# Kernel tuning notes

Hardware: AMD Instinct MI355X
Metric: run time of the kernel (lower is better)

Reference implementation:

```python
import jax, jax.numpy as jnp
import numpy as np

WS = (2, 8, 8)      # window size (wt, wh, ww)
SS = (1, 4, 4)      # shift size
HEADS = 6


def _window_partition(x, ws):
    B, T, H, W, C = x.shape
    wt, wh, ww = ws
    x = x.reshape(B, T // wt, wt, H // wh, wh, W // ww, ww, C)
    x = x.transpose(0, 1, 3, 5, 2, 4, 6, 7)
    return x.reshape(-1, wt * wh * ww, C)  # (B*nW, N, C)


def _window_reverse(w, ws, B, T, H, W):
    wt, wh, ww = ws
    C = w.shape[-1]
    x = w.reshape(B, T // wt, H // wh, W // ww, wt, wh, ww, C)
    x = x.transpose(0, 1, 4, 2, 5, 3, 6, 7)
    return x.reshape(B, T, H, W, C)


def _rel_pos_index(ws):
    wt, wh, ww = ws
    coords = np.stack(np.meshgrid(np.arange(wt), np.arange(wh), np.arange(ww), indexing='ij'))
    coords = coords.reshape(3, -1)                      # (3, N)
    rel = coords[:, :, None] - coords[:, None, :]       # (3, N, N)
    rel = rel.transpose(1, 2, 0).astype(np.int32)
    rel[..., 0] += wt - 1
    rel[..., 1] += wh - 1
    rel[..., 2] += ww - 1
    rel[..., 0] *= (2 * wh - 1) * (2 * ww - 1)
    rel[..., 1] *= (2 * ww - 1)
    return rel.sum(-1)                                  # (N, N)


def _shift_mask(T, H, W, ws, ss):
    # standard Swin shifted-window attention mask
    img = np.zeros((1, T, H, W, 1), dtype=np.float32)
    cnt = 0
    for t in (slice(0, -ws[0]), slice(-ws[0], -ss[0]), slice(-ss[0], None)):
        for h in (slice(0, -ws[1]), slice(-ws[1], -ss[1]), slice(-ss[1], None)):
            for w in (slice(0, -ws[2]), slice(-ws[2], -ss[2]), slice(-ss[2], None)):
                img[:, t, h, w, :] = cnt
                cnt += 1
    mw = np.asarray(_window_partition(jnp.asarray(img), ws)).squeeze(-1)  # (nW, N)
    diff = mw[:, None, :] - mw[:, :, None]
    return jnp.asarray(np.where(diff != 0, -100.0, 0.0).astype(np.float32))


def setup_inputs() -> dict:
    key = jax.random.key(0)
    ks = jax.random.split(key, 9)
    B, T, H, W, C = 2, 8, 64, 64, 192
    hid = 4 * C
    s = 0.02
    x = jax.random.normal(ks[0], (B, T, H, W, C), jnp.float32)
    qkv_w = jax.random.normal(ks[1], (3 * C, C), jnp.float32) * s
    qkv_b = jnp.zeros((3 * C,), jnp.float32)
    proj_w = jax.random.normal(ks[2], (C, C), jnp.float32) * s
    proj_b = jnp.zeros((C,), jnp.float32)
    n_rel = (2 * WS[0] - 1) * (2 * WS[1] - 1) * (2 * WS[2] - 1)
    rpb_table = jax.random.normal(ks[3], (n_rel, HEADS), jnp.float32) * s
    rpb_index = jnp.asarray(_rel_pos_index(WS))
    fc1_w = jax.random.normal(ks[4], (hid, C), jnp.float32) * s
    fc1_b = jnp.zeros((hid,), jnp.float32)
    fc2_w = jax.random.normal(ks[5], (C, hid), jnp.float32) * s
    fc2_b = jnp.zeros((C,), jnp.float32)
    attn_mask = _shift_mask(T, H, W, WS, SS)
    return dict(x=x, attn_mask=attn_mask, qkv_w=qkv_w, qkv_b=qkv_b, proj_w=proj_w,
                proj_b=proj_b, rpb_table=rpb_table, rpb_index=rpb_index,
                fc1_w=fc1_w, fc1_b=fc1_b, fc2_w=fc2_w, fc2_b=fc2_b)


def reference(x, attn_mask, qkv_w, qkv_b, proj_w, proj_b, rpb_table, rpb_index,
              fc1_w, fc1_b, fc2_w, fc2_b):
    B, T, H, W, C = x.shape
    h = HEADS
    d = C // h
    scale = d ** -0.5

    shifted = jnp.roll(x, (-SS[0], -SS[1], -SS[2]), axis=(1, 2, 3))
    xw = _window_partition(shifted, WS)            # (Bn, N, C)
    Bn, N, _ = xw.shape

    qkv = (xw @ qkv_w.T + qkv_b).reshape(Bn, N, 3, h, d).transpose(2, 0, 3, 1, 4)
    q, k, v = qkv[0], qkv[1], qkv[2]               # (Bn, h, N, d)
    attn = jnp.einsum('bhnd,bhmd->bhnm', q * scale, k)
    bias = rpb_table[rpb_index.reshape(-1)].reshape(N, N, h).transpose(2, 0, 1)
    attn = attn + bias[None]
    nW = attn_mask.shape[0]
    attn = (attn.reshape(Bn // nW, nW, h, N, N) + attn_mask[None, :, None]).reshape(Bn, h, N, N)
    attn = jax.nn.softmax(attn, axis=-1)
    out = jnp.einsum('bhnm,bhmd->bhnd', attn, v).transpose(0, 2, 1, 3).reshape(Bn, N, C)
    out = out @ proj_w.T + proj_b

    z = _window_reverse(out, WS, B, T, H, W)
    z = jnp.roll(z, (SS[0], SS[1], SS[2]), axis=(1, 2, 3))

    y = z + x
    mlp = jax.nn.gelu(y @ fc1_w.T + fc1_b, approximate=False) @ fc2_w.T + fc2_b
    return x + mlp
```

## Files before the change

### kernel.cpp

```cpp
#include <hip/hip_runtime.h>
#include <hip/hip_bf16.h>

typedef __attribute__((ext_vector_type(4))) float f32x4;
typedef __attribute__((ext_vector_type(8))) short bf16x8;

#define DEV __device__ __forceinline__

DEV unsigned short f2bf(float f) {
  union { float f; unsigned int u; } v; v.f = f;
  unsigned int r = v.u + 0x7fffu + ((v.u >> 16) & 1u);
  return (unsigned short)(r >> 16);
}

DEV float bf2f(unsigned short u) {
  union { unsigned int u; float f; } v; v.u = ((unsigned int)u) << 16; return v.f;
}

DEV short2 pkbf(float a, float b) {
  float2 t; t.x = a; t.y = b;
  __hip_bfloat162 h = __float22bfloat162_rn(t);
  union { __hip_bfloat162 h; short2 s; } u; u.h = h; return u.s;
}

DEV bf16x8 cvt8(float4 u, float4 v) {
  short2 a = pkbf(u.x, u.y), b = pkbf(u.z, u.w), c = pkbf(v.x, v.y), d = pkbf(v.z, v.w);
  bf16x8 r;
  r[0] = a.x; r[1] = a.y; r[2] = b.x; r[3] = b.y;
  r[4] = c.x; r[5] = c.y; r[6] = d.x; r[7] = d.y;
  return r;
}

DEV float gelu_fast(float v) {
  float u = 1.5957691216057308f * v * (1.0f + 0.044715f * v * v);
  return v * __builtin_amdgcn_rcpf(1.0f + __expf(-u));
}

DEV size_t winmap(int row) {
  int wIdx = row >> 7, n = row & 127;
  int b = wIdx >> 8, widx = wIdx & 255;
  int t = (((widx >> 6) * 2 + (n >> 6)) + 1) & 7;
  int h = ((((widx >> 3) & 7) * 8 + ((n >> 3) & 7)) + 4) & 63;
  int w = (((widx & 7) * 8 + (n & 7)) + 4) & 63;
  return (size_t)(((b * 8 + t) * 64 + h) * 64 + w);
}

DEV int reg3(int tw, int hw, int ww, int n) {
  int ts = tw * 2 + (n >> 6);
  int hs = hw * 8 + ((n >> 3) & 7);
  int wsv = ww * 8 + (n & 7);
  int rt = (ts >= 7) ? 2 : ((ts >= 6) ? 1 : 0);
  int rh = (hs >= 60) ? 2 : ((hs >= 56) ? 1 : 0);
  int rw = (wsv >= 60) ? 2 : ((wsv >= 56) ? 1 : 0);
  return rt * 9 + rh * 3 + rw;
}

DEV void gload16(const unsigned short* g, unsigned short* lds) {
  __builtin_amdgcn_global_load_lds(
      (const __attribute__((address_space(1))) unsigned int*)g,
      (__attribute__((address_space(3))) unsigned int*)lds, 16, 0, 0);
}

__global__ __launch_bounds__(256) void k_prep(
    const float* __restrict__ qkv_w, const float* __restrict__ proj_w,
    const float* __restrict__ fc1_w, const float* __restrict__ fc2_w,
    const float* __restrict__ rpb_t, const int* __restrict__ rpb_i,
    unsigned short* __restrict__ wq, unsigned short* __restrict__ wp,
    unsigned short* __restrict__ w1, unsigned short* __restrict__ w2,
    float* __restrict__ b6) {
  int i = blockIdx.x * 256 + threadIdx.x;
  if (i < 110592) wq[i] = f2bf(qkv_w[i]);
  if (i < 36864)  wp[i] = f2bf(proj_w[i]);
  if (i < 147456) { w1[i] = f2bf(fc1_w[i]); w2[i] = f2bf(fc2_w[i]); }
  if (i < 16384) {
    int row = i >> 7, col = i & 127;
    int idx = rpb_i[i];
    int dest = (row >> 4) * 2048 + (((row >> 2) & 3) * 16 + (col & 15)) * 32 +
               (col >> 4) * 4 + (row & 3);
    #pragma unroll
    for (int h = 0; h < 6; ++h) b6[h * 16384 + dest] = rpb_t[idx * 6 + h];
  }
}

__global__ __launch_bounds__(256) void k_qkv(
    const float* __restrict__ x, const unsigned short* __restrict__ Bm,
    const float* __restrict__ bias, unsigned short* __restrict__ outb) {
  __shared__ char smem[40960];
  float* As = (float*)smem;
  unsigned short* Bs = (unsigned short*)(smem + 32768);
  unsigned short* Cs = (unsigned short*)smem;
  const int tid = threadIdx.x;
  const int wave = tid >> 6, lane = tid & 63;
  const int lin = ((int)blockIdx.x & 7) * 576 + ((int)blockIdx.x >> 3);
  const int mt = lin / 9, nt = lin - mt * 9;
  const int m0 = mt * 128, n0 = nt * 64;
  const int wr = wave >> 1, wc = wave & 1;
  const int l8 = lane >> 3, s8 = lane & 7;

  const float* aptr[8];
  #pragma unroll
  for (int i = 0; i < 8; ++i) {
    int row = wave * 32 + i * 4 + (lane >> 4);
    aptr[i] = x + winmap(m0 + row) * 192 + (((lane & 15) ^ (row & 15)) << 2);
  }

  f32x4 acc[4][2] = {};
  for (int kt = 0; kt < 192; kt += 64) {
    __syncthreads();
    #pragma unroll
    for (int i = 0; i < 8; ++i)
      gload16((const unsigned short*)(aptr[i] + kt), (unsigned short*)(As + (wave * 8 + i) * 256));
    #pragma unroll
    for (int j = 0; j < 2; ++j) {
      int c = wave * 2 + j;
      int row = c * 8 + l8;
      gload16(Bm + (size_t)(n0 + row) * 192 + kt + (s8 ^ l8) * 8, Bs + c * 512);
    }
    __syncthreads();

    #pragma unroll
    for (int kk = 0; kk < 2; ++kk) {
      bf16x8 af[4], bfr[2];
      #pragma unroll
      for (int mi = 0; mi < 4; ++mi) {
        int r = wr * 64 + mi * 16 + (lane & 15);
        int s0 = kk * 8 + (lane >> 4) * 2;
        float4 u = *(const float4*)(As + r * 64 + ((s0 ^ (r & 15)) << 2));
        float4 v = *(const float4*)(As + r * 64 + (((s0 + 1) ^ (r & 15)) << 2));
        af[mi] = cvt8(u, v);
      }
      #pragma unroll
      for (int ni = 0; ni < 2; ++ni) {
        int row = wc * 32 + ni * 16 + (lane & 15);
        int slot = (kk * 4 + (lane >> 4)) ^ (row & 7);
        bfr[ni] = *(const bf16x8*)(Bs + row * 64 + slot * 8);
      }
      #pragma unroll
      for (int mi = 0; mi < 4; ++mi)
        #pragma unroll
        for (int ni = 0; ni < 2; ++ni)
          acc[mi][ni] = __builtin_amdgcn_mfma_f32_16x16x32_bf16(af[mi], bfr[ni], acc[mi][ni], 0, 0, 0);
    }
  }

  __syncthreads();
  #pragma unroll
  for (int ni = 0; ni < 2; ++ni) {
    int coll = wc * 32 + ni * 16 + (lane & 15);
    float bb = bias[n0 + coll];
    #pragma unroll
    for (int mi = 0; mi < 4; ++mi) {
      int rbase = wr * 64 + mi * 16 + ((lane >> 4) << 2);
      #pragma unroll
      for (int j = 0; j < 4; ++j)
        Cs[(rbase + j) * 72 + coll] = f2bf(acc[mi][ni][j] + bb);
    }
  }
  __syncthreads();
  const int row = tid >> 1, hh = tid & 1;
  unsigned short* gb = outb + (size_t)(m0 + row) * 576 + n0 + hh * 32;
  #pragma unroll
  for (int s = 0; s < 4; ++s)
    *(bf16x8*)(gb + s * 8) = *(const bf16x8*)(Cs + row * 72 + hh * 32 + s * 8);
}

DEV void stage_head(const unsigned short* qkv, size_t qbase, int h,
                    const unsigned short* wp, unsigned short* Kl,
                    unsigned short* Vt, unsigned short* Wp,
                    int tid, int wave, int lane) {
  {
    int row = tid >> 2, slot = tid & 3;
    int m = (row + (row >> 2)) & 3;
    *(bf16x8*)(Kl + row * 32 + ((slot ^ m) * 8)) =
        *(const bf16x8*)(qkv + qbase + (size_t)row * 576 + 192 + h * 32 + slot * 8);
  }
  {
    int vtok = tid & 127, slot = tid >> 7;
    bf16x8 v = *(const bf16x8*)(qkv + qbase + (size_t)vtok * 576 + 384 + h * 32 + slot * 8);
    #pragma unroll
    for (int j = 0; j < 8; ++j) Vt[(slot * 8 + j) * 136 + vtok] = (unsigned short)v[j];
  }
  {
    int c = wave;
    int rg = c * 16 + (lane >> 2);
    gload16(wp + (size_t)rg * 192 + h * 32 + (((lane & 3) ^ ((rg >> 1) & 3)) * 8), Wp + c * 512);
    if (wave < 4) {
      int c2 = 8 + wave;
      int rg2 = c2 * 16 + (lane >> 2);
      gload16(wp + (size_t)rg2 * 192 + h * 32 + (((lane & 3) ^ ((rg2 >> 1) & 3)) * 8), Wp + c2 * 512);
    }
  }
}

__global__ __launch_bounds__(512, 4) void k_attnproj(
    const unsigned short* __restrict__ qkv, const float* __restrict__ bias6,
    const unsigned short* __restrict__ wp, const float* __restrict__ proj_b,
    const float* __restrict__ x, unsigned short* __restrict__ ybf) {
  __shared__ unsigned short Kl[128 * 32];
  __shared__ unsigned short Vt[32 * 136];
  __shared__ unsigned short Pl[128 * 140];
  __shared__ unsigned short Os[128 * 40];
  __shared__ unsigned short Wp[192 * 32];
  const int tid = threadIdx.x;
  const int wave = tid >> 6, lane = tid & 63;
  const int lrow = lane & 15, lk = lane >> 4;
  const int wIdx = ((int)blockIdx.x & 7) * 64 + ((int)blockIdx.x >> 3);
  const int widx = wIdx & 255;
  const int tw = widx >> 6, hw = (widx >> 3) & 7, ww = widx & 7;
  const size_t qbase = (size_t)wIdx * 73728;
  const float scale = 0.17677669529663687f;

  int rcol[8];
  #pragma unroll
  for (int tc = 0; tc < 8; ++tc) rcol[tc] = reg3(tw, hw, ww, tc * 16 + lrow);
  int rreg[4];
  #pragma unroll
  for (int j = 0; j < 4; ++j) rreg[j] = reg3(tw, hw, ww, wave * 16 + lk * 4 + j);

  bf16x8 ones;
  #pragma unroll
  for (int j = 0; j < 8; ++j) ones[j] = (short)0x3F80;

  stage_head(qkv, qbase, 0, wp, Kl, Vt, Wp, tid, wave, lane);

  f32x4 oaccP[12] = {};
  for (int h = 0; h < 6; ++h) {
    __syncthreads();

    bf16x8 qf = *(const bf16x8*)(qkv + qbase + (size_t)(wave * 16 + lrow) * 576 +
                                 h * 32 + lk * 8);
    f32x4 s[8];
    #pragma unroll
    for (int tc = 0; tc < 8; ++tc) {
      int krow = tc * 16 + lrow;
      int m = (krow + (krow >> 2)) & 3;
      bf16x8 kf = *(const bf16x8*)(Kl + krow * 32 + ((lk ^ m) * 8));
      f32x4 z = {0.f, 0.f, 0.f, 0.f};
      s[tc] = __builtin_amdgcn_mfma_f32_16x16x32_bf16(qf, kf, z, 0, 0, 0);
    }

    {
      const float* bp = bias6 + h * 16384 + wave * 2048 + lane * 32;
      f32x4 bb[8];
      #pragma unroll
      for (int tc = 0; tc < 8; ++tc) bb[tc] = *(const f32x4*)(bp + tc * 4);
      #pragma unroll
      for (int tc = 0; tc < 8; ++tc) {
        #pragma unroll
        for (int j = 0; j < 4; ++j) {
          float v = fmaf(s[tc][j], scale,
                         bb[tc][j] + ((rreg[j] == rcol[tc]) ? 0.0f : -100.0f));
          int row = wave * 16 + lk * 4 + j;
          Pl[row * 140 + tc * 16 + lrow] = f2bf(__expf(v));
        }
      }
    }

    f32x4 o[2] = {};
    f32x4 osum = {};
    #pragma unroll
    for (int ks = 0; ks < 4; ++ks) {
      bf16x8 pa = *(const bf16x8*)(Pl + (wave * 16 + lrow) * 140 + ks * 32 + lk * 8);
      #pragma unroll
      for (int nc = 0; nc < 2; ++nc) {
        bf16x8 vb = *(const bf16x8*)(Vt + (nc * 16 + lrow) * 136 + ks * 32 + lk * 8);
        o[nc] = __builtin_amdgcn_mfma_f32_16x16x32_bf16(pa, vb, o[nc], 0, 0, 0);
      }
      osum = __builtin_amdgcn_mfma_f32_16x16x32_bf16(pa, ones, osum, 0, 0, 0);
    }
    #pragma unroll
    for (int j = 0; j < 4; ++j) {
      float rinv = __builtin_amdgcn_rcpf(osum[j]);
      int row = wave * 16 + lk * 4 + j;
      #pragma unroll
      for (int nc = 0; nc < 2; ++nc)
        Os[row * 40 + nc * 16 + lrow] = f2bf(o[nc][j] * rinv);
    }

    {
      bf16x8 af = *(const bf16x8*)(Os + (wave * 16 + lrow) * 40 + lk * 8);
      #pragma unroll
      for (int ni = 0; ni < 12; ++ni) {
        int n = ni * 16 + lrow;
        bf16x8 bv = *(const bf16x8*)(Wp + n * 32 + ((lk ^ ((n >> 1) & 3)) * 8));
        oaccP[ni] = __builtin_amdgcn_mfma_f32_16x16x32_bf16(af, bv, oaccP[ni], 0, 0, 0);
      }
    }
    __syncthreads();
    if (h < 5) stage_head(qkv, qbase, h + 1, wp, Kl, Vt, Wp, tid, wave, lane);
  }

  size_t gf[4];
  #pragma unroll
  for (int j = 0; j < 4; ++j)
    gf[j] = winmap(wIdx * 128 + wave * 16 + lk * 4 + j) * 192;
  #pragma unroll
  for (int ni = 0; ni < 12; ++ni) {
    int col = ni * 16 + lrow;
    float bb = proj_b[col];
    #pragma unroll
    for (int j = 0; j < 4; ++j) {
      size_t idx = gf[j] + col;
      ybf[idx] = f2bf(oaccP[ni][j] + bb + x[idx]);
    }
  }
}

DEV void stage_w(const unsigned short* w1, const unsigned short* w2, int hb,
                 char* smem, int buf, int wave, int lane) {
  unsigned short* d1 = (unsigned short*)(smem + buf * 12288);
  unsigned short* d2 = (unsigned short*)(smem + 24576 + buf * 12288);
  const int l8 = lane >> 3, s8 = lane & 7;
  {
    int c = wave, p = c >> 2, q = c & 3;
    gload16(w1 + (size_t)(hb + q * 8 + l8) * 192 + p * 64 + ((s8 ^ l8) * 8), d1 + c * 512);
  }
  if (wave < 4) {
    int c = 8 + wave, p = c >> 2, q = c & 3;
    gload16(w1 + (size_t)(hb + q * 8 + l8) * 192 + p * 64 + ((s8 ^ l8) * 8), d1 + c * 512);
  }
  {
    int c = wave;
    int rg = c * 16 + (lane >> 2);
    gload16(w2 + (size_t)rg * 768 + hb + (((lane & 3) ^ ((rg >> 1) & 3)) * 8), d2 + c * 512);
  }
  if (wave < 4) {
    int c = 8 + wave;
    int rg = c * 16 + (lane >> 2);
    gload16(w2 + (size_t)rg * 768 + hb + (((lane & 3) ^ ((rg >> 1) & 3)) * 8), d2 + c * 512);
  }
}

__global__ __launch_bounds__(512, 4) void k_mlp(
    const unsigned short* __restrict__ y, const unsigned short* __restrict__ w1,
    const float* __restrict__ b1, const unsigned short* __restrict__ w2,
    const float* __restrict__ b2, const float* __restrict__ xin,
    float* __restrict__ out) {
  __shared__ char smem[57344];
  unsigned short* Hs = (unsigned short*)(smem + 49152);
  const int tid = threadIdx.x;
  const int wave = tid >> 6, lane = tid & 63;
  const int lrow = lane & 15, lk = lane >> 4;
  const int m0 = (int)blockIdx.x * 128;
  const int tok = wave * 16 + lrow;
  const int tq = (lrow >> 1) & 3;

  bf16x8 yfr[6];
  {
    const unsigned short* yp = y + (size_t)(m0 + tok) * 192 + lk * 8;
    #pragma unroll
    for (int kk = 0; kk < 6; ++kk) yfr[kk] = *(const bf16x8*)(yp + kk * 32);
  }

  stage_w(w1, w2, 0, smem, 0, wave, lane);
  stage_w(w1, w2, 32, smem, 1, wave, lane);
  __syncthreads();

  f32x4 oacc[12] = {};
  for (int c = 0; c < 24; ++c) {
    const int hb = c * 32;
    unsigned short* w1b = (unsigned short*)(smem + (c & 1) * 12288);
    unsigned short* w2b = (unsigned short*)(smem + 24576 + (c & 1) * 12288);

    f32x4 hacc[2] = {};
    #pragma unroll
    for (int kk = 0; kk < 6; ++kk) {
      int p = kk >> 1, sc = (kk & 1) * 4;
      #pragma unroll
      for (int hi = 0; hi < 2; ++hi) {
        bf16x8 av = *(const bf16x8*)(w1b + p * 2048 + (hi * 16 + lrow) * 64 +
                                     (((sc + lk) ^ (lrow & 7)) * 8));
        hacc[hi] = __builtin_amdgcn_mfma_f32_16x16x32_bf16(av, yfr[kk], hacc[hi], 0, 0, 0);
      }
    }

    #pragma unroll
    for (int hi = 0; hi < 2; ++hi) {
      float4 bb = *(const float4*)(b1 + hb + hi * 16 + lk * 4);
      short2 p01 = pkbf(gelu_fast(hacc[hi][0] + bb.x), gelu_fast(hacc[hi][1] + bb.y));
      short2 p23 = pkbf(gelu_fast(hacc[hi][2] + bb.z), gelu_fast(hacc[hi][3] + bb.w));
      ushort4 o;
      o.x = (unsigned short)p01.x; o.y = (unsigned short)p01.y;
      o.z = (unsigned short)p23.x; o.w = (unsigned short)p23.y;
      int g = hi * 4 + lk;
      *(ushort4*)(Hs + tok * 32 + (((g >> 1) ^ tq) * 8) + (g & 1) * 4) = o;
    }

    {
      bf16x8 af = *(const bf16x8*)(Hs + tok * 32 + ((lk ^ tq) * 8));
      #pragma unroll
      for (int ni = 0; ni < 12; ++ni) {
        int n = ni * 16 + lrow;
        bf16x8 bv = *(const bf16x8*)(w2b + n * 32 + ((lk ^ ((n >> 1) & 3)) * 8));
        oacc[ni] = __builtin_amdgcn_mfma_f32_16x16x32_bf16(af, bv, oacc[ni], 0, 0, 0);
      }
    }

    __syncthreads();
    if (c < 22) stage_w(w1, w2, hb + 64, smem, c & 1, wave, lane);
  }

  #pragma unroll
  for (int ni = 0; ni < 12; ++ni) {
    int col = ni * 16 + lrow;
    float bb = b2[col];
    #pragma unroll
    for (int j = 0; j < 4; ++j) {
      size_t idx = (size_t)(m0 + wave * 16 + lk * 4 + j) * 192 + col;
      out[idx] = xin[idx] + oacc[ni][j] + bb;
    }
  }
}

extern "C" void kernel_launch(void* const* d_in, const int* in_sizes, int n_in,
                              void* d_out, int out_size, void* d_ws, size_t ws_size,
                              hipStream_t stream) {
  const float* x      = (const float*)d_in[0];
  const float* qkv_w  = (const float*)d_in[2];
  const float* qkv_b  = (const float*)d_in[3];
  const float* proj_w = (const float*)d_in[4];
  const float* proj_b = (const float*)d_in[5];
  const float* rpb_t  = (const float*)d_in[6];
  const int*   rpb_i  = (const int*)d_in[7];
  const float* fc1_w  = (const float*)d_in[8];
  const float* fc1_b  = (const float*)d_in[9];
  const float* fc2_w  = (const float*)d_in[10];
  const float* fc2_b  = (const float*)d_in[11];
  float* out = (float*)d_out;
  char* ws = (char*)d_ws;

  unsigned short* qkv = (unsigned short*)(ws + 0);
  unsigned short* ybf = (unsigned short*)(ws + 100663296);
  unsigned short* wq  = (unsigned short*)(ws + 125829120);
  unsigned short* wp  = (unsigned short*)(ws + 126050304);
  unsigned short* w1  = (unsigned short*)(ws + 126124032);
  unsigned short* w2  = (unsigned short*)(ws + 126418944);
  float*          b6  = (float*)(ws + 126713856);

  k_prep<<<576, 256, 0, stream>>>(qkv_w, proj_w, fc1_w, fc2_w, rpb_t, rpb_i, wq, wp, w1, w2, b6);
  k_qkv<<<4608, 256, 0, stream>>>(x, wq, qkv_b, qkv);
  k_attnproj<<<512, 512, 0, stream>>>(qkv, b6, wp, proj_b, x, ybf);
  k_mlp<<<512, 512, 0, stream>>>(ybf, w1, fc1_b, w2, fc2_b, x, out);
}
```

Measured before the change: 176.1 us.

## Keep attention probabilities in registers via transposed MFMA and lane shuffles

Computes S^T (K as the A operand, Q as B) so each lane holds scores for one query row. Probabilities are exponentiated, packed to bf16 and redistributed with cross-lane shuffles into the B operand of the PV MFMA, which removes the Pl LDS buffer and its stores and reloads. The row sum now comes from a register accumulation plus xor-shuffles instead of an extra MFMA against a ones vector. The shift-mask comparison is precomputed as a 32-bit bitmask, and the bias table layout is permuted to match the transposed fragments. Shuffles add VALU/DS work, and the results stay correct only if the permuted bias layout matches the new fragment mapping exactly.

```diff
diff --git a/kernel.cpp b/kernel.cpp
--- a/kernel.cpp
+++ b/kernel.cpp
@@ -20,6 +20,10 @@
   float2 t; t.x = a; t.y = b;
   __hip_bfloat162 h = __float22bfloat162_rn(t);
   union { __hip_bfloat162 h; short2 s; } u; u.h = h; return u.s;
+}
+
+DEV int pk2i(float a, float b) {
+  union { short2 s; int i; } u; u.s = pkbf(a, b); return u.i;
 }
 
 DEV bf16x8 cvt8(float4 u, float4 v) {
@@ -72,10 +76,10 @@
   if (i < 36864)  wp[i] = f2bf(proj_w[i]);
   if (i < 147456) { w1[i] = f2bf(fc1_w[i]); w2[i] = f2bf(fc2_w[i]); }
   if (i < 16384) {
-    int row = i >> 7, col = i & 127;
+    int q = i >> 7, col = i & 127;
     int idx = rpb_i[i];
-    int dest = (row >> 4) * 2048 + (((row >> 2) & 3) * 16 + (col & 15)) * 32 +
-               (col >> 4) * 4 + (row & 3);
+    int dest = (q >> 4) * 2048 + ((col >> 2) & 3) * 512 + (q & 15) * 32 +
+               (col >> 4) * 4 + (col & 3);
     #pragma unroll
     for (int h = 0; h < 6; ++h) b6[h * 16384 + dest] = rpb_t[idx * 6 + h];
   }
@@ -197,7 +201,6 @@
     const float* __restrict__ x, unsigned short* __restrict__ ybf) {
   __shared__ unsigned short Kl[128 * 32];
   __shared__ unsigned short Vt[32 * 136];
-  __shared__ unsigned short Pl[128 * 140];
   __shared__ unsigned short Os[128 * 40];
   __shared__ unsigned short Wp[192 * 32];
   const int tid = threadIdx.x;
@@ -209,16 +212,13 @@
   const size_t qbase = (size_t)wIdx * 73728;
   const float scale = 0.17677669529663687f;
 
-  int rcol[8];
-  #pragma unroll
-  for (int tc = 0; tc < 8; ++tc) rcol[tc] = reg3(tw, hw, ww, tc * 16 + lrow);
-  int rreg[4];
-  #pragma unroll
-  for (int j = 0; j < 4; ++j) rreg[j] = reg3(tw, hw, ww, wave * 16 + lk * 4 + j);
-
-  bf16x8 ones;
-  #pragma unroll
-  for (int j = 0; j < 8; ++j) ones[j] = (short)0x3F80;
+  const int rq = reg3(tw, hw, ww, wave * 16 + lrow);
+  unsigned int mbits = 0;
+  #pragma unroll
+  for (int tc = 0; tc < 8; ++tc)
+    #pragma unroll
+    for (int j = 0; j < 4; ++j)
+      mbits |= (unsigned int)(reg3(tw, hw, ww, 16 * tc + 4 * lk + j) == rq) << (tc * 4 + j);
 
   stage_head(qkv, qbase, 0, wp, Kl, Vt, Wp, tid, wave, lane);
 
@@ -228,52 +228,68 @@
 
     bf16x8 qf = *(const bf16x8*)(qkv + qbase + (size_t)(wave * 16 + lrow) * 576 +
                                  h * 32 + lk * 8);
-    f32x4 s[8];
-    #pragma unroll
-    for (int tc = 0; tc < 8; ++tc) {
-      int krow = tc * 16 + lrow;
-      int m = (krow + (krow >> 2)) & 3;
-      bf16x8 kf = *(const bf16x8*)(Kl + krow * 32 + ((lk ^ m) * 8));
-      f32x4 z = {0.f, 0.f, 0.f, 0.f};
-      s[tc] = __builtin_amdgcn_mfma_f32_16x16x32_bf16(qf, kf, z, 0, 0, 0);
-    }
-
-    {
-      const float* bp = bias6 + h * 16384 + wave * 2048 + lane * 32;
-      f32x4 bb[8];
-      #pragma unroll
-      for (int tc = 0; tc < 8; ++tc) bb[tc] = *(const f32x4*)(bp + tc * 4);
-      #pragma unroll
-      for (int tc = 0; tc < 8; ++tc) {
-        #pragma unroll
-        for (int j = 0; j < 4; ++j) {
-          float v = fmaf(s[tc][j], scale,
-                         bb[tc][j] + ((rreg[j] == rcol[tc]) ? 0.0f : -100.0f));
-          int row = wave * 16 + lk * 4 + j;
-          Pl[row * 140 + tc * 16 + lrow] = f2bf(__expf(v));
-        }
-      }
-    }
+    const float* bp = bias6 + h * 16384 + wave * 2048 + lane * 32;
 
     f32x4 o[2] = {};
-    f32x4 osum = {};
+    float psum = 0.f;
     #pragma unroll
     for (int ks = 0; ks < 4; ++ks) {
-      bf16x8 pa = *(const bf16x8*)(Pl + (wave * 16 + lrow) * 140 + ks * 32 + lk * 8);
+      f32x4 s0, s1;
+      {
+        int kr0 = (2 * ks) * 16 + lrow;
+        int m0s = (kr0 + (kr0 >> 2)) & 3;
+        bf16x8 kf0 = *(const bf16x8*)(Kl + kr0 * 32 + ((lk ^ m0s) * 8));
+        int kr1 = (2 * ks + 1) * 16 + lrow;
+        int m1s = (kr1 + (kr1 >> 2)) & 3;
+        bf16x8 kf1 = *(const bf16x8*)(Kl + kr1 * 32 + ((lk ^ m1s) * 8));
+        f32x4 z = {0.f, 0.f, 0.f, 0.f};
+        s0 = __builtin_amdgcn_mfma_f32_16x16x32_bf16(kf0, qf, z, 0, 0, 0);
+        s1 = __builtin_amdgcn_mfma_f32_16x16x32_bf16(kf1, qf, z, 0, 0, 0);
+      }
+      f32x4 bb0 = *(const f32x4*)(bp + (2 * ks) * 4);
+      f32x4 bb1 = *(const f32x4*)(bp + (2 * ks + 1) * 4);
+      #pragma unroll
+      for (int j = 0; j < 4; ++j) {
+        float m0v = ((mbits >> ((2 * ks) * 4 + j)) & 1) ? 0.0f : -100.0f;
+        float m1v = ((mbits >> ((2 * ks + 1) * 4 + j)) & 1) ? 0.0f : -100.0f;
+        s0[j] = __expf(fmaf(s0[j], scale, bb0[j] + m0v));
+        s1[j] = __expf(fmaf(s1[j], scale, bb1[j] + m1v));
+        psum += s0[j] + s1[j];
+      }
+      int A0 = pk2i(s0[0], s0[1]), A1 = pk2i(s0[2], s0[3]);
+      int B0 = pk2i(s1[0], s1[1]), B1 = pk2i(s1[2], s1[3]);
+      int base = (lk & 1) * 32 + lrow;
+      int w0u = __shfl(A0, base),      w0v = __shfl(B0, base);
+      int w1u = __shfl(A1, base),      w1v = __shfl(B1, base);
+      int w2u = __shfl(A0, base + 16), w2v = __shfl(B0, base + 16);
+      int w3u = __shfl(A1, base + 16), w3v = __shfl(B1, base + 16);
+      union { int w[4]; bf16x8 v; } pb;
+      int hi = lk >> 1;
+      pb.w[0] = hi ? w0v : w0u;
+      pb.w[1] = hi ? w1v : w1u;
+      pb.w[2] = hi ? w2v : w2u;
+      pb.w[3] = hi ? w3v : w3u;
       #pragma unroll
       for (int nc = 0; nc < 2; ++nc) {
         bf16x8 vb = *(const bf16x8*)(Vt + (nc * 16 + lrow) * 136 + ks * 32 + lk * 8);
-        o[nc] = __builtin_amdgcn_mfma_f32_16x16x32_bf16(pa, vb, o[nc], 0, 0, 0);
-      }
-      osum = __builtin_amdgcn_mfma_f32_16x16x32_bf16(pa, ones, osum, 0, 0, 0);
-    }
-    #pragma unroll
-    for (int j = 0; j < 4; ++j) {
-      float rinv = __builtin_amdgcn_rcpf(osum[j]);
-      int row = wave * 16 + lk * 4 + j;
-      #pragma unroll
-      for (int nc = 0; nc < 2; ++nc)
-        Os[row * 40 + nc * 16 + lrow] = f2bf(o[nc][j] * rinv);
+        o[nc] = __builtin_amdgcn_mfma_f32_16x16x32_bf16(vb, pb.v, o[nc], 0, 0, 0);
+      }
+    }
+    psum += __shfl_xor(psum, 16);
+    psum += __shfl_xor(psum, 32);
+    float rinv = __builtin_amdgcn_rcpf(psum);
+
+    {
+      int qrow = wave * 16 + lrow;
+      #pragma unroll
+      for (int nc = 0; nc < 2; ++nc) {
+        short2 a = pkbf(o[nc][0] * rinv, o[nc][1] * rinv);
+        short2 b = pkbf(o[nc][2] * rinv, o[nc][3] * rinv);
+        ushort4 ov;
+        ov.x = (unsigned short)a.x; ov.y = (unsigned short)a.y;
+        ov.z = (unsigned short)b.x; ov.w = (unsigned short)b.y;
+        *(ushort4*)(Os + qrow * 40 + nc * 16 + lk * 4) = ov;
+      }
     }
 
     {
```

After: 179.8 us. 2.1% more time.
